# Performance work log

Measured on AMD Instinct MI355X. Metric: run time of the kernel, lower is better.

The kernel has to match this reference:

```python
import jax, jax.numpy as jnp
import numpy as np

N, D, K, V, H, F_ = 4096, 128, 64, 64, 4, 256
EPS = 1e-5


def _layer_norm(x, g, b):
    m = jnp.mean(x, axis=-1, keepdims=True)
    v = jnp.mean((x - m) ** 2, axis=-1, keepdims=True)
    return (x - m) * jax.lax.rsqrt(v + EPS) * g + b


def setup_inputs() -> dict:
    key = jax.random.key(0)
    ks = jax.random.split(key, 20)
    s_in = (2.0 / D) ** 0.5  # kaiming-ish scale for q/k/v projections
    inp = {
        "x": jax.random.normal(ks[0], (N, D), jnp.float32),
        "rpe": jax.random.normal(ks[1], (5, N, N), jnp.float32) * 0.02,
        "Wq": jax.random.normal(ks[2], (H, D, K), jnp.float32) * s_in,
        "bq": jnp.zeros((H, K), jnp.float32),
        "Wk": jax.random.normal(ks[3], (H, D, K), jnp.float32) * s_in,
        "bk": jnp.zeros((H, K), jnp.float32),
        "Wv": jax.random.normal(ks[4], (H, D, V), jnp.float32) * s_in,
        "bv": jnp.zeros((H, V), jnp.float32),
        "rpe_w": jax.random.normal(ks[5], (5,), jnp.float32) * (1.0 / 5.0) ** 0.5,
        "rpe_b": jnp.zeros((), jnp.float32),
        "Wo": jax.random.normal(ks[6], (H * V, D), jnp.float32) * (1.0 / (H * V)) ** 0.5,
        "bo": jnp.zeros((D,), jnp.float32),
        "W1": jax.random.normal(ks[7], (D, F_), jnp.float32) * (1.0 / D) ** 0.5,
        "b1": jnp.zeros((F_,), jnp.float32),
        "W2": jax.random.normal(ks[8], (F_, D), jnp.float32) * (1.0 / F_) ** 0.5,
        "b2": jnp.zeros((D,), jnp.float32),
        "ln1_g": jnp.ones((D,), jnp.float32),
        "ln1_b": jnp.zeros((D,), jnp.float32),
        "ln2_g": jnp.ones((D,), jnp.float32),
        "ln2_b": jnp.zeros((D,), jnp.float32),
    }
    return inp


def reference(x, rpe, Wq, bq, Wk, bk, Wv, bv, rpe_w, rpe_b, Wo, bo,
              W1, b1, W2, b2, ln1_g, ln1_b, ln2_g, ln2_b):
    # ReLU'd per-head projections (vectorized over heads): [H, N, K/V]
    q = jax.nn.relu(jnp.einsum("nd,hdk->hnk", x, Wq) + bq[:, None, :])
    k = jax.nn.relu(jnp.einsum("nd,hdk->hnk", x, Wk) + bk[:, None, :])
    v = jax.nn.relu(jnp.einsum("nd,hdv->hnv", x, Wv) + bv[:, None, :])
    scores = jnp.einsum("hnk,hmk->hnm", q, k) / jnp.sqrt(jnp.asarray(K, x.dtype))
    attn = jax.nn.softmax(scores, axis=-1)  # torch dim=1 on 2D == last axis
    o = jnp.einsum("hnm,hmv->hnv", attn, v)
    mho = jnp.transpose(o, (1, 0, 2)).reshape(N, H * V)  # concat heads
    # RPE: Linear(5->1) over channel axis -> [N, N], then left-matmul
    rpe_weights = jnp.einsum("fnm,f->nm", rpe, rpe_w) + rpe_b
    adjusted = rpe_weights @ mho
    proj = adjusted @ Wo + bo
    x1 = _layer_norm(x + proj, ln1_g, ln1_b)  # dropout is identity (eval)
    ffn = jax.nn.relu(x1 @ W1 + b1) @ W2 + b2
    return _layer_norm(x1 + ffn, ln2_g, ln2_b)
```

## Files before the change

kernel.cpp:

```cpp
#include <hip/hip_runtime.h>

typedef __attribute__((ext_vector_type(8))) short bf16x8;
typedef __attribute__((ext_vector_type(4))) float f32x4;

#define N_TOK 4096
#define NC_ATT 4
#define NC_GEMM 8

static __device__ __forceinline__ ushort f2bf(float f) {
    union { float f; unsigned u; } x; x.f = f;
    unsigned u = x.u;
    unsigned r = (u + 0x7FFFu + ((u >> 16) & 1u)) >> 16;
    return (ushort)r;
}
static __device__ __forceinline__ unsigned pkbf(float a, float b) {
    return (unsigned)f2bf(a) | ((unsigned)f2bf(b) << 16);
}

__global__ void prep_all(const float* __restrict__ x,
                         const float* __restrict__ Wq, const float* __restrict__ Wk,
                         const float* __restrict__ Wv, const float* __restrict__ Wo,
                         const float* __restrict__ W1, const float* __restrict__ W2,
                         ushort* __restrict__ xb, ushort* __restrict__ WqT,
                         ushort* __restrict__ WkT, ushort* __restrict__ WvT,
                         ushort* __restrict__ WoT, ushort* __restrict__ W1T,
                         ushort* __restrict__ W2T) {
    int i = blockIdx.x * 256 + threadIdx.x;
    if (i < 131072) {
        float4 v = ((const float4*)x)[i];
        ushort4 o;
        o.x = f2bf(v.x); o.y = f2bf(v.y); o.z = f2bf(v.z); o.w = f2bf(v.w);
        ((ushort4*)xb)[i] = o;
        return;
    }
    int j = i - 131072;
    int t = j >> 15, e = j & 32767;
    if (t < 3) {
        const float* src = (t == 0 ? Wq : t == 1 ? Wk : Wv);
        ushort* dst = (t == 0 ? WqT : t == 1 ? WkT : WvT);
        int h = e >> 13, rem = e & 8191, d = rem >> 6, k = rem & 63;
        dst[h * 8192 + k * 128 + d] = f2bf(src[e]);
    } else if (t == 3) {
        int r = e >> 7, c = e & 127;
        WoT[c * 256 + r] = f2bf(Wo[e]);
    } else if (t == 4) {
        int r = e >> 8, c = e & 255;
        W1T[c * 128 + r] = f2bf(W1[e]);
    } else {
        int r = e >> 7, c = e & 127;
        W2T[c * 256 + r] = f2bf(W2[e]);
    }
}

__global__ __launch_bounds__(256) void qkv_proj(
    const ushort* __restrict__ xb, const ushort* __restrict__ WqT,
    const ushort* __restrict__ WkT, const ushort* __restrict__ WvT,
    const float* __restrict__ bq, const float* __restrict__ bk, const float* __restrict__ bv,
    ushort* __restrict__ qb, ushort* __restrict__ kb, ushort* __restrict__ vT) {
    int m0 = blockIdx.x * 64;
    int h = blockIdx.y & 3, which = blockIdx.y >> 2;
    int wave = threadIdx.x >> 6, lane = threadIdx.x & 63;
    int fr = lane & 15, kg = lane >> 4;
    int wm = m0 + wave * 16;
    const ushort* WT = (which == 0 ? WqT : which == 1 ? WkT : WvT) + (long)h * 64 * 128;
    const float* bias = (which == 0 ? bq : which == 1 ? bk : bv) + h * 64;
    f32x4 acc[4] = {};
    for (int k0 = 0; k0 < 128; k0 += 32) {
        bf16x8 a = *(const bf16x8*)(xb + (long)(wm + fr) * 128 + k0 + kg * 8);
#pragma unroll
        for (int t = 0; t < 4; ++t) {
            bf16x8 b = *(const bf16x8*)(WT + (long)(t * 16 + fr) * 128 + k0 + kg * 8);
            acc[t] = __builtin_amdgcn_mfma_f32_16x16x32_bf16(a, b, acc[t], 0, 0, 0);
        }
    }
    int rb = wm + kg * 4;
#pragma unroll
    for (int t = 0; t < 4; ++t) {
        int col = t * 16 + fr;
        float bs = bias[col];
        if (which == 2) {
            ushort4 o;
            o.x = f2bf(fmaxf(acc[t][0] + bs, 0.f));
            o.y = f2bf(fmaxf(acc[t][1] + bs, 0.f));
            o.z = f2bf(fmaxf(acc[t][2] + bs, 0.f));
            o.w = f2bf(fmaxf(acc[t][3] + bs, 0.f));
            *(ushort4*)(vT + ((long)h * 64 + col) * N_TOK + rb) = o;
        } else {
            ushort* dst = (which == 0 ? qb : kb) + (long)h * N_TOK * 64;
            float scl = (which == 0) ? 0.125f : 1.0f;
#pragma unroll
            for (int r = 0; r < 4; ++r)
                dst[(long)(rb + r) * 64 + col] = f2bf(fmaxf(acc[t][r] + bs, 0.f) * scl);
        }
    }
}

__global__ __launch_bounds__(256) void attn_flash2(
    const ushort* __restrict__ qb, const ushort* __restrict__ kb,
    const ushort* __restrict__ vT, float* __restrict__ opart,
    float* __restrict__ mlpart) {
    int qt = blockIdx.x, h = blockIdx.y, cz = blockIdx.z;
    int w = threadIdx.x >> 6, lane = threadIdx.x & 63;
    int fr = lane & 15, kg = lane >> 4;
    int lr = lane >> 3, lc = lane & 7;
    int swz = (lc ^ (lr & 7)) * 8;
    __shared__ ushort Kt[2][64 * 64];
    __shared__ ushort Vt[2][64 * 64];
    __shared__ ushort Pl[4][16 * 64];
    const ushort* qh = qb + (long)h * N_TOK * 64;
    const ushort* kh = kb + (long)h * N_TOK * 64;
    const ushort* vh = vT + (long)h * 64 * N_TOK;
    int q0 = qt * 64 + w * 16;
    bf16x8 qf0 = *(const bf16x8*)(qh + (long)(q0 + fr) * 64 + kg * 8);
    bf16x8 qf1 = *(const bf16x8*)(qh + (long)(q0 + fr) * 64 + 32 + kg * 8);
    f32x4 o[4] = {};
    float mrun = -1e30f, lrun = 0.f;
    int nbase = cz * (N_TOK / NC_ATT);
    auto stage = [&](int buf, int s) {
        int n0 = nbase + s * 64;
#pragma unroll
        for (int j = 0; j < 2; ++j) {
            int i = w * 2 + j;
            int row = i * 8 + lr;
            __builtin_amdgcn_global_load_lds(
                (const __attribute__((address_space(1))) unsigned int*)(kh + (long)(n0 + row) * 64 + swz),
                (__attribute__((address_space(3))) unsigned int*)(&Kt[buf][i * 512]), 16, 0, 0);
        }
#pragma unroll
        for (int j = 0; j < 2; ++j) {
            int i = w * 2 + j;
            int row = i * 8 + lr;
            __builtin_amdgcn_global_load_lds(
                (const __attribute__((address_space(1))) unsigned int*)(vh + (long)row * N_TOK + n0 + swz),
                (__attribute__((address_space(3))) unsigned int*)(&Vt[buf][i * 512]), 16, 0, 0);
        }
    };
    stage(0, 0);
    __syncthreads();
    const int NS = (N_TOK / NC_ATT) / 64;
    for (int s = 0; s < NS; ++s) {
        int buf = s & 1;
        if (s + 1 < NS) stage(buf ^ 1, s + 1);
        f32x4 sc[4] = {};
#pragma unroll
        for (int t = 0; t < 4; ++t) {
            int row = t * 16 + fr;
            bf16x8 k0 = *(const bf16x8*)(&Kt[buf][row * 64 + ((kg * 8) ^ ((row & 7) * 8))]);
            bf16x8 k1 = *(const bf16x8*)(&Kt[buf][row * 64 + ((32 + kg * 8) ^ ((row & 7) * 8))]);
            sc[t] = __builtin_amdgcn_mfma_f32_16x16x32_bf16(k0, qf0, sc[t], 0, 0, 0);
            sc[t] = __builtin_amdgcn_mfma_f32_16x16x32_bf16(k1, qf1, sc[t], 0, 0, 0);
        }
        float mx = sc[0][0];
#pragma unroll
        for (int t = 0; t < 4; ++t)
#pragma unroll
            for (int r = 0; r < 4; ++r) mx = fmaxf(mx, sc[t][r]);
        mx = fmaxf(mx, __shfl_xor(mx, 16));
        mx = fmaxf(mx, __shfl_xor(mx, 32));
        float mnew = fmaxf(mrun, mx);
        float alpha = __expf(mrun - mnew);
        float rs = 0.f;
#pragma unroll
        for (int t = 0; t < 4; ++t)
#pragma unroll
            for (int r = 0; r < 4; ++r) {
                float p = __expf(sc[t][r] - mnew);
                sc[t][r] = p;
                rs += p;
            }
        rs += __shfl_xor(rs, 16);
        rs += __shfl_xor(rs, 32);
        lrun = lrun * alpha + rs;
        mrun = mnew;
        float aq[4];
#pragma unroll
        for (int r = 0; r < 4; ++r) aq[r] = __shfl(alpha, kg * 4 + r);
#pragma unroll
        for (int t = 0; t < 4; ++t)
#pragma unroll
            for (int r = 0; r < 4; ++r) o[t][r] *= aq[r];
#pragma unroll
        for (int t = 0; t < 4; ++t) {
            uint2 u;
            u.x = pkbf(sc[t][0], sc[t][1]);
            u.y = pkbf(sc[t][2], sc[t][3]);
            *(uint2*)(&Pl[w][fr * 64 + ((t * 16 + kg * 4) ^ ((fr & 7) * 8))]) = u;
        }
#pragma unroll
        for (int ks = 0; ks < 2; ++ks) {
            bf16x8 pf = *(const bf16x8*)(&Pl[w][fr * 64 + ((ks * 32 + kg * 8) ^ ((fr & 7) * 8))]);
#pragma unroll
            for (int t = 0; t < 4; ++t) {
                int row = t * 16 + fr;
                bf16x8 b = *(const bf16x8*)(&Vt[buf][row * 64 + ((ks * 32 + kg * 8) ^ ((row & 7) * 8))]);
                o[t] = __builtin_amdgcn_mfma_f32_16x16x32_bf16(pf, b, o[t], 0, 0, 0);
            }
        }
        __syncthreads();
    }
    float linv = 1.0f / lrun;
    float lq[4];
#pragma unroll
    for (int r = 0; r < 4; ++r) lq[r] = __shfl(linv, kg * 4 + r);
    float* ob = opart + (((long)cz * 4 + h) * N_TOK + q0 + kg * 4) * 64;
#pragma unroll
    for (int t = 0; t < 4; ++t)
#pragma unroll
        for (int r = 0; r < 4; ++r)
            ob[(long)r * 64 + t * 16 + fr] = o[t][r] * lq[r];
    if (lane < 16) {
        float* mlb = mlpart + (((long)cz * 4 + h) * N_TOK + q0 + lane) * 2;
        mlb[0] = mrun;
        mlb[1] = lrun;
    }
}

__global__ __launch_bounds__(256) void attn_combine(
    const float* __restrict__ opart, const float* __restrict__ mlpart,
    ushort* __restrict__ mho) {
    int h = blockIdx.y;
    int q0 = blockIdx.x * 64;
    int tid = threadIdx.x;
    int ql = tid >> 4, qv = tid & 15;
#pragma unroll
    for (int pass = 0; pass < 4; ++pass) {
        int q = q0 + pass * 16 + ql;
        float m[NC_ATT], l[NC_ATT], M = -1e30f;
#pragma unroll
        for (int c = 0; c < NC_ATT; ++c) {
            const float* mlb = mlpart + (((long)c * 4 + h) * N_TOK + q) * 2;
            m[c] = mlb[0]; l[c] = mlb[1];
            M = fmaxf(M, m[c]);
        }
        float L = 0.f, wgt[NC_ATT];
#pragma unroll
        for (int c = 0; c < NC_ATT; ++c) { wgt[c] = __expf(m[c] - M); L += l[c] * wgt[c]; }
        float inv = 1.0f / L;
#pragma unroll
        for (int c = 0; c < NC_ATT; ++c) wgt[c] *= l[c] * inv;
        float ax = 0.f, ay = 0.f, az = 0.f, aw = 0.f;
#pragma unroll
        for (int c = 0; c < NC_ATT; ++c) {
            float4 v = *(const float4*)(opart + (((long)c * 4 + h) * N_TOK + q) * 64 + qv * 4);
            ax += v.x * wgt[c]; ay += v.y * wgt[c]; az += v.z * wgt[c]; aw += v.w * wgt[c];
        }
        ushort4 o;
        o.x = f2bf(ax); o.y = f2bf(ay); o.z = f2bf(az); o.w = f2bf(aw);
        *(ushort4*)(mho + (long)q * 256 + h * 64 + qv * 4) = o;
    }
}

__global__ __launch_bounds__(256) void gemm_bt_plain(
    const ushort* __restrict__ A, const ushort* __restrict__ BT,
    ushort* __restrict__ outp, int Ncols, int Kd) {
    int m0 = blockIdx.x * 64, n0 = blockIdx.y * 64;
    int wave = threadIdx.x >> 6, lane = threadIdx.x & 63;
    int fr = lane & 15, kg = lane >> 4;
    int wm = m0 + wave * 16;
    f32x4 acc[4] = {};
    for (int k0 = 0; k0 < Kd; k0 += 32) {
        bf16x8 a = *(const bf16x8*)(A + (long)(wm + fr) * Kd + k0 + kg * 8);
#pragma unroll
        for (int t = 0; t < 4; ++t) {
            bf16x8 b = *(const bf16x8*)(BT + (long)(n0 + t * 16 + fr) * Kd + k0 + kg * 8);
            acc[t] = __builtin_amdgcn_mfma_f32_16x16x32_bf16(a, b, acc[t], 0, 0, 0);
        }
    }
    int rb = wm + kg * 4;
#pragma unroll
    for (int t = 0; t < 4; ++t) {
        int col = n0 + t * 16 + fr;
#pragma unroll
        for (int r = 0; r < 4; ++r)
            outp[(long)(rb + r) * Ncols + col] = f2bf(acc[t][r]);
    }
}

__global__ __launch_bounds__(512) void gemm_big_fused(
    const float* __restrict__ rpe, const float* __restrict__ rpe_w,
    const float* __restrict__ rpe_b, const ushort* __restrict__ PT,
    float* __restrict__ part) {
    int mt = blockIdx.x, cz = blockIdx.y;
    int tid = threadIdx.x;
    int w = tid >> 6, lane = tid & 63;
    int fr = lane & 15, kg = lane >> 4;
    int lr = lane >> 3, lc = lane & 7;
    int swz = (lc ^ (lr & 7)) * 8;
    int ms = w >> 1, nh = w & 1;
    __shared__ ushort Bt[2][128 * 64];
    __shared__ ushort At[2][64 * 64];
    int m0 = mt * 64;
    long kbase = (long)cz * (N_TOK / NC_GEMM);
    float w0 = rpe_w[0], w1 = rpe_w[1], w2 = rpe_w[2], w3 = rpe_w[3], w4 = rpe_w[4];
    float bb = rpe_b[0];
    auto stage_B = [&](int buf, int s) {
        const ushort* src = PT + kbase + s * 64 + swz;
#pragma unroll
        for (int j = 0; j < 2; ++j) {
            int i = w * 2 + j;
            int row = i * 8 + lr;
            __builtin_amdgcn_global_load_lds(
                (const __attribute__((address_space(1))) unsigned int*)(src + (long)row * N_TOK),
                (__attribute__((address_space(3))) unsigned int*)(&Bt[buf][i * 512]), 16, 0, 0);
        }
    };
    float4 pA[10];
    auto load_A = [&](int s) {
        const float* base = rpe + (long)m0 * N_TOK + kbase + s * 64;
#pragma unroll
        for (int rnd = 0; rnd < 2; ++rnd) {
            int idx = tid + rnd * 512;
            int row = idx >> 4, c4 = (idx & 15) * 4;
            const float* pr = base + (long)row * N_TOK + c4;
#pragma unroll
            for (int pl = 0; pl < 5; ++pl)
                pA[rnd * 5 + pl] = *(const float4*)(pr + (long)pl * ((long)N_TOK * N_TOK));
        }
    };
    auto write_A = [&](int buf) {
#pragma unroll
        for (int rnd = 0; rnd < 2; ++rnd) {
            int idx = tid + rnd * 512;
            int row = idx >> 4, c4 = (idx & 15) * 4;
            float4 p0 = pA[rnd * 5], p1 = pA[rnd * 5 + 1], p2 = pA[rnd * 5 + 2];
            float4 p3 = pA[rnd * 5 + 3], p4 = pA[rnd * 5 + 4];
            float v0 = bb + w0 * p0.x + w1 * p1.x + w2 * p2.x + w3 * p3.x + w4 * p4.x;
            float v1 = bb + w0 * p0.y + w1 * p1.y + w2 * p2.y + w3 * p3.y + w4 * p4.y;
            float v2 = bb + w0 * p0.z + w1 * p1.z + w2 * p2.z + w3 * p3.z + w4 * p4.z;
            float v3 = bb + w0 * p0.w + w1 * p1.w + w2 * p2.w + w3 * p3.w + w4 * p4.w;
            uint2 u;
            u.x = pkbf(v0, v1);
            u.y = pkbf(v2, v3);
            *(uint2*)(&At[buf][row * 64 + (c4 ^ ((row & 7) * 8))]) = u;
        }
    };
    f32x4 acc[4] = {};
    load_A(0);
    stage_B(0, 0);
    write_A(0);
    __syncthreads();
    const int NS = (N_TOK / NC_GEMM) / 64;
    int arow = ms * 16 + fr;
    for (int s = 0; s < NS; ++s) {
        int buf = s & 1;
        if (s + 1 < NS) { stage_B(buf ^ 1, s + 1); load_A(s + 1); }
#pragma unroll
        for (int ks = 0; ks < 2; ++ks) {
            bf16x8 av = *(const bf16x8*)(&At[buf][arow * 64 + ((ks * 32 + kg * 8) ^ ((arow & 7) * 8))]);
#pragma unroll
            for (int nf = 0; nf < 4; ++nf) {
                int row = nh * 64 + nf * 16 + fr;
                bf16x8 b = *(const bf16x8*)(&Bt[buf][row * 64 + ((ks * 32 + kg * 8) ^ ((row & 7) * 8))]);
                acc[nf] = __builtin_amdgcn_mfma_f32_16x16x32_bf16(av, b, acc[nf], 0, 0, 0);
            }
        }
        if (s + 1 < NS) write_A(buf ^ 1);
        __syncthreads();
    }
    float* pb = part + ((long)cz * N_TOK + m0 + ms * 16 + kg * 4) * 128 + nh * 64 + fr;
#pragma unroll
    for (int nf = 0; nf < 4; ++nf)
#pragma unroll
        for (int r = 0; r < 4; ++r)
            pb[(long)r * 128 + nf * 16] = acc[nf][r];
}

__global__ __launch_bounds__(256) void megatail(
    const float* __restrict__ gpart, const float* __restrict__ bo,
    const float* __restrict__ x, const float* __restrict__ g1,
    const float* __restrict__ lb1, const ushort* __restrict__ W1T,
    const float* __restrict__ b1, const ushort* __restrict__ W2T,
    const float* __restrict__ b2, const float* __restrict__ g2,
    const float* __restrict__ lb2, float* __restrict__ out) {
    int r0 = blockIdx.x * 16;
    int tid = threadIdx.x;
    int w = tid >> 6, lane = tid & 63;
    int fr = lane & 15, kg = lane >> 4;
    __shared__ float x1f[16][132];
    __shared__ ushort x1b[16][128];
    __shared__ ushort hbuf[16][256];
    __shared__ float otile[16][132];
    int row = tid >> 4, c0 = (tid & 15) * 8;
    {
        float v[8];
        float4 s0 = {0.f, 0.f, 0.f, 0.f}, s1 = {0.f, 0.f, 0.f, 0.f};
#pragma unroll
        for (int c = 0; c < NC_GEMM; ++c) {
            const float* pr = gpart + ((long)c * N_TOK + r0 + row) * 128 + c0;
            float4 a = *(const float4*)(pr);
            float4 b = *(const float4*)(pr + 4);
            s0.x += a.x; s0.y += a.y; s0.z += a.z; s0.w += a.w;
            s1.x += b.x; s1.y += b.y; s1.z += b.z; s1.w += b.w;
        }
        const float* xr = x + (long)(r0 + row) * 128 + c0;
        v[0] = s0.x + bo[c0 + 0] + xr[0];
        v[1] = s0.y + bo[c0 + 1] + xr[1];
        v[2] = s0.z + bo[c0 + 2] + xr[2];
        v[3] = s0.w + bo[c0 + 3] + xr[3];
        v[4] = s1.x + bo[c0 + 4] + xr[4];
        v[5] = s1.y + bo[c0 + 5] + xr[5];
        v[6] = s1.z + bo[c0 + 6] + xr[6];
        v[7] = s1.w + bo[c0 + 7] + xr[7];
        float s = 0.f;
#pragma unroll
        for (int jj = 0; jj < 8; ++jj) s += v[jj];
#pragma unroll
        for (int off = 1; off < 16; off <<= 1) s += __shfl_xor(s, off);
        float mean = s * (1.0f / 128.0f);
        float ss = 0.f;
#pragma unroll
        for (int jj = 0; jj < 8; ++jj) { float d = v[jj] - mean; ss += d * d; }
#pragma unroll
        for (int off = 1; off < 16; off <<= 1) ss += __shfl_xor(ss, off);
        float rstd = rsqrtf(ss * (1.0f / 128.0f) + 1e-5f);
        union { bf16x8 vec; ushort us[8]; } pk8;
#pragma unroll
        for (int jj = 0; jj < 8; ++jj) {
            float y = (v[jj] - mean) * rstd * g1[c0 + jj] + lb1[c0 + jj];
            x1f[row][c0 + jj] = y;
            pk8.us[jj] = f2bf(y);
        }
        *(bf16x8*)(&x1b[row][c0 ^ ((row & 7) * 8)]) = pk8.vec;
    }
    __syncthreads();
    {
        f32x4 a1[4] = {};
#pragma unroll
        for (int ks = 0; ks < 4; ++ks) {
            bf16x8 a = *(const bf16x8*)(&x1b[fr][(ks * 32 + kg * 8) ^ ((fr & 7) * 8)]);
#pragma unroll
            for (int t = 0; t < 4; ++t) {
                bf16x8 b = *(const bf16x8*)(W1T + (long)(w * 64 + t * 16 + fr) * 128 + ks * 32 + kg * 8);
                a1[t] = __builtin_amdgcn_mfma_f32_16x16x32_bf16(a, b, a1[t], 0, 0, 0);
            }
        }
#pragma unroll
        for (int t = 0; t < 4; ++t) {
            int col = w * 64 + t * 16 + fr;
            float bs = b1[col];
#pragma unroll
            for (int r = 0; r < 4; ++r) {
                int rr = kg * 4 + r;
                hbuf[rr][col ^ ((rr & 7) * 8)] = f2bf(fmaxf(a1[t][r] + bs, 0.f));
            }
        }
    }
    __syncthreads();
    {
        f32x4 a2[2] = {};
#pragma unroll
        for (int ks = 0; ks < 8; ++ks) {
            bf16x8 a = *(const bf16x8*)(&hbuf[fr][(ks * 32 + kg * 8) ^ ((fr & 7) * 8)]);
#pragma unroll
            for (int t = 0; t < 2; ++t) {
                bf16x8 b = *(const bf16x8*)(W2T + (long)(w * 32 + t * 16 + fr) * 256 + ks * 32 + kg * 8);
                a2[t] = __builtin_amdgcn_mfma_f32_16x16x32_bf16(a, b, a2[t], 0, 0, 0);
            }
        }
#pragma unroll
        for (int t = 0; t < 2; ++t) {
            int col = w * 32 + t * 16 + fr;
            float bs = b2[col];
#pragma unroll
            for (int r = 0; r < 4; ++r) {
                int rr = kg * 4 + r;
                otile[rr][col] = a2[t][r] + bs + x1f[rr][col];
            }
        }
    }
    __syncthreads();
    {
        float v[8];
        float s = 0.f;
#pragma unroll
        for (int jj = 0; jj < 8; ++jj) { v[jj] = otile[row][c0 + jj]; s += v[jj]; }
#pragma unroll
        for (int off = 1; off < 16; off <<= 1) s += __shfl_xor(s, off);
        float mean = s * (1.0f / 128.0f);
        float ss = 0.f;
#pragma unroll
        for (int jj = 0; jj < 8; ++jj) { float d = v[jj] - mean; ss += d * d; }
#pragma unroll
        for (int off = 1; off < 16; off <<= 1) ss += __shfl_xor(ss, off);
        float rstd = rsqrtf(ss * (1.0f / 128.0f) + 1e-5f);
#pragma unroll
        for (int jj = 0; jj < 8; ++jj) {
            float y = (v[jj] - mean) * rstd * g2[c0 + jj] + lb2[c0 + jj];
            out[(long)(r0 + row) * 128 + c0 + jj] = y;
        }
    }
}

extern "C" void kernel_launch(void* const* d_in, const int* in_sizes, int n_in,
                              void* d_out, int out_size, void* d_ws, size_t ws_size,
                              hipStream_t stream) {
    const float* x     = (const float*)d_in[0];
    const float* rpe   = (const float*)d_in[1];
    const float* Wq    = (const float*)d_in[2];
    const float* bq    = (const float*)d_in[3];
    const float* Wk    = (const float*)d_in[4];
    const float* bk    = (const float*)d_in[5];
    const float* Wv    = (const float*)d_in[6];
    const float* bv    = (const float*)d_in[7];
    const float* rpe_w = (const float*)d_in[8];
    const float* rpe_b = (const float*)d_in[9];
    const float* Wo    = (const float*)d_in[10];
    const float* bo    = (const float*)d_in[11];
    const float* W1    = (const float*)d_in[12];
    const float* b1    = (const float*)d_in[13];
    const float* W2    = (const float*)d_in[14];
    const float* b2    = (const float*)d_in[15];
    const float* g1    = (const float*)d_in[16];
    const float* lb1   = (const float*)d_in[17];
    const float* g2    = (const float*)d_in[18];
    const float* lb2   = (const float*)d_in[19];

    char* wp = (char*)d_ws;
    auto alloc = [&](size_t sz) { char* p = wp; wp += (sz + 255) & ~(size_t)255; return p; };
    ushort* xb    = (ushort*)alloc((size_t)4096 * 128 * 2);
    ushort* WqT   = (ushort*)alloc((size_t)4 * 64 * 128 * 2);
    ushort* WkT   = (ushort*)alloc((size_t)4 * 64 * 128 * 2);
    ushort* WvT   = (ushort*)alloc((size_t)4 * 64 * 128 * 2);
    ushort* WoT   = (ushort*)alloc((size_t)128 * 256 * 2);
    ushort* W1T   = (ushort*)alloc((size_t)256 * 128 * 2);
    ushort* W2T   = (ushort*)alloc((size_t)128 * 256 * 2);
    ushort* qb    = (ushort*)alloc((size_t)4 * 4096 * 64 * 2);
    ushort* kbuf  = (ushort*)alloc((size_t)4 * 4096 * 64 * 2);
    ushort* vT    = (ushort*)alloc((size_t)4 * 64 * 4096 * 2);
    ushort* mho   = (ushort*)alloc((size_t)4096 * 256 * 2);
    ushort* PTb   = (ushort*)alloc((size_t)128 * 4096 * 2);
    float*  opart = (float*)alloc((size_t)NC_ATT * 4 * 4096 * 64 * 4);
    float*  mlprt = (float*)alloc((size_t)NC_ATT * 4 * 4096 * 2 * 4);
    float*  gpart = (float*)alloc((size_t)NC_GEMM * 4096 * 128 * 4);

    prep_all<<<1280, 256, 0, stream>>>(x, Wq, Wk, Wv, Wo, W1, W2,
                                       xb, WqT, WkT, WvT, WoT, W1T, W2T);
    qkv_proj<<<dim3(64, 12), 256, 0, stream>>>(xb, WqT, WkT, WvT, bq, bk, bv, qb, kbuf, vT);
    attn_flash2<<<dim3(64, 4, NC_ATT), 256, 0, stream>>>(qb, kbuf, vT, opart, mlprt);
    attn_combine<<<dim3(64, 4), 256, 0, stream>>>(opart, mlprt, mho);
    gemm_bt_plain<<<dim3(2, 64), 256, 0, stream>>>(WoT, mho, PTb, 4096, 256);
    gemm_big_fused<<<dim3(64, NC_GEMM), 512, 0, stream>>>(rpe, rpe_w, rpe_b, PTb, gpart);
    megatail<<<256, 256, 0, stream>>>(gpart, bo, x, g1, lb1, W1T, b1, W2T, b2,
                                      g2, lb2, (float*)d_out);
}
```

Measured before the change: 152.4 us.

## Fuse attention combine with Wo projection, store partials in bf16, lazy rescale

The attention split-combine and the Wo projection GEMM are merged into one kernel. It combines the per-chunk partials into a swizzled LDS tile and runs the MFMA against WoT directly, so the intermediate mho buffer and one launch go away. Attention partial outputs are now stored as bf16 instead of fp32, halving that traffic. The flash loop folds log2(e) into the q scale to use exp2f, and only rescales the accumulators when the running max grows by more than 8. This trades some precision (bf16 partials, p values up to 2^8) for fewer exp and multiply operations.

```diff
diff --git a/kernel.cpp b/kernel.cpp
--- a/kernel.cpp
+++ b/kernel.cpp
@@ -15,6 +15,9 @@
 }
 static __device__ __forceinline__ unsigned pkbf(float a, float b) {
     return (unsigned)f2bf(a) | ((unsigned)f2bf(b) << 16);
+}
+static __device__ __forceinline__ float bf2f(ushort u) {
+    union { unsigned u; float f; } x; x.u = (unsigned)u << 16; return x.f;
 }
 
 __global__ void prep_all(const float* __restrict__ x,
@@ -87,7 +90,7 @@
             *(ushort4*)(vT + ((long)h * 64 + col) * N_TOK + rb) = o;
         } else {
             ushort* dst = (which == 0 ? qb : kb) + (long)h * N_TOK * 64;
-            float scl = (which == 0) ? 0.125f : 1.0f;
+            float scl = (which == 0) ? 0.125f * 1.44269504f : 1.0f;
 #pragma unroll
             for (int r = 0; r < 4; ++r)
                 dst[(long)(rb + r) * 64 + col] = f2bf(fmaxf(acc[t][r] + bs, 0.f) * scl);
@@ -97,7 +100,7 @@
 
 __global__ __launch_bounds__(256) void attn_flash2(
     const ushort* __restrict__ qb, const ushort* __restrict__ kb,
-    const ushort* __restrict__ vT, float* __restrict__ opart,
+    const ushort* __restrict__ vT, ushort* __restrict__ opart,
     float* __restrict__ mlpart) {
     int qt = blockIdx.x, h = blockIdx.y, cz = blockIdx.z;
     int w = threadIdx.x >> 6, lane = threadIdx.x & 63;
@@ -157,28 +160,31 @@
             for (int r = 0; r < 4; ++r) mx = fmaxf(mx, sc[t][r]);
         mx = fmaxf(mx, __shfl_xor(mx, 16));
         mx = fmaxf(mx, __shfl_xor(mx, 32));
-        float mnew = fmaxf(mrun, mx);
-        float alpha = __expf(mrun - mnew);
+        if (__any(mx - mrun > 8.f)) {
+            float mnew = fmaxf(mrun, mx);
+            float alpha = exp2f(mrun - mnew);
+            lrun *= alpha;
+            mrun = mnew;
+            float aq[4];
+#pragma unroll
+            for (int r = 0; r < 4; ++r) aq[r] = __shfl(alpha, kg * 4 + r);
+#pragma unroll
+            for (int t = 0; t < 4; ++t)
+#pragma unroll
+                for (int r = 0; r < 4; ++r) o[t][r] *= aq[r];
+        }
         float rs = 0.f;
 #pragma unroll
         for (int t = 0; t < 4; ++t)
 #pragma unroll
             for (int r = 0; r < 4; ++r) {
-                float p = __expf(sc[t][r] - mnew);
+                float p = exp2f(sc[t][r] - mrun);
                 sc[t][r] = p;
                 rs += p;
             }
         rs += __shfl_xor(rs, 16);
         rs += __shfl_xor(rs, 32);
-        lrun = lrun * alpha + rs;
-        mrun = mnew;
-        float aq[4];
-#pragma unroll
-        for (int r = 0; r < 4; ++r) aq[r] = __shfl(alpha, kg * 4 + r);
-#pragma unroll
-        for (int t = 0; t < 4; ++t)
-#pragma unroll
-            for (int r = 0; r < 4; ++r) o[t][r] *= aq[r];
+        lrun += rs;
 #pragma unroll
         for (int t = 0; t < 4; ++t) {
             uint2 u;
@@ -202,12 +208,12 @@
     float lq[4];
 #pragma unroll
     for (int r = 0; r < 4; ++r) lq[r] = __shfl(linv, kg * 4 + r);
-    float* ob = opart + (((long)cz * 4 + h) * N_TOK + q0 + kg * 4) * 64;
+    ushort* ob = opart + (((long)cz * 4 + h) * N_TOK + q0 + kg * 4) * 64;
 #pragma unroll
     for (int t = 0; t < 4; ++t)
 #pragma unroll
         for (int r = 0; r < 4; ++r)
-            ob[(long)r * 64 + t * 16 + fr] = o[t][r] * lq[r];
+            ob[(long)r * 64 + t * 16 + fr] = f2bf(o[t][r] * lq[r]);
     if (lane < 16) {
         float* mlb = mlpart + (((long)cz * 4 + h) * N_TOK + q0 + lane) * 2;
         mlb[0] = mrun;
@@ -215,64 +221,80 @@
     }
 }
 
-__global__ __launch_bounds__(256) void attn_combine(
-    const float* __restrict__ opart, const float* __restrict__ mlpart,
-    ushort* __restrict__ mho) {
-    int h = blockIdx.y;
+__global__ __launch_bounds__(256) void combine_wo(
+    const ushort* __restrict__ opart, const float* __restrict__ mlpart,
+    const ushort* __restrict__ WoT, ushort* __restrict__ PT) {
     int q0 = blockIdx.x * 64;
     int tid = threadIdx.x;
-    int ql = tid >> 4, qv = tid & 15;
-#pragma unroll
-    for (int pass = 0; pass < 4; ++pass) {
-        int q = q0 + pass * 16 + ql;
-        float m[NC_ATT], l[NC_ATT], M = -1e30f;
-#pragma unroll
-        for (int c = 0; c < NC_ATT; ++c) {
-            const float* mlb = mlpart + (((long)c * 4 + h) * N_TOK + q) * 2;
-            m[c] = mlb[0]; l[c] = mlb[1];
-            M = fmaxf(M, m[c]);
-        }
-        float L = 0.f, wgt[NC_ATT];
-#pragma unroll
-        for (int c = 0; c < NC_ATT; ++c) { wgt[c] = __expf(m[c] - M); L += l[c] * wgt[c]; }
-        float inv = 1.0f / L;
-#pragma unroll
-        for (int c = 0; c < NC_ATT; ++c) wgt[c] *= l[c] * inv;
-        float ax = 0.f, ay = 0.f, az = 0.f, aw = 0.f;
-#pragma unroll
-        for (int c = 0; c < NC_ATT; ++c) {
-            float4 v = *(const float4*)(opart + (((long)c * 4 + h) * N_TOK + q) * 64 + qv * 4);
-            ax += v.x * wgt[c]; ay += v.y * wgt[c]; az += v.z * wgt[c]; aw += v.w * wgt[c];
-        }
-        ushort4 o;
-        o.x = f2bf(ax); o.y = f2bf(ay); o.z = f2bf(az); o.w = f2bf(aw);
-        *(ushort4*)(mho + (long)q * 256 + h * 64 + qv * 4) = o;
-    }
-}
-
-__global__ __launch_bounds__(256) void gemm_bt_plain(
-    const ushort* __restrict__ A, const ushort* __restrict__ BT,
-    ushort* __restrict__ outp, int Ncols, int Kd) {
-    int m0 = blockIdx.x * 64, n0 = blockIdx.y * 64;
-    int wave = threadIdx.x >> 6, lane = threadIdx.x & 63;
-    int fr = lane & 15, kg = lane >> 4;
-    int wm = m0 + wave * 16;
-    f32x4 acc[4] = {};
-    for (int k0 = 0; k0 < Kd; k0 += 32) {
-        bf16x8 a = *(const bf16x8*)(A + (long)(wm + fr) * Kd + k0 + kg * 8);
-#pragma unroll
-        for (int t = 0; t < 4; ++t) {
-            bf16x8 b = *(const bf16x8*)(BT + (long)(n0 + t * 16 + fr) * Kd + k0 + kg * 8);
-            acc[t] = __builtin_amdgcn_mfma_f32_16x16x32_bf16(a, b, acc[t], 0, 0, 0);
-        }
-    }
-    int rb = wm + kg * 4;
-#pragma unroll
-    for (int t = 0; t < 4; ++t) {
-        int col = n0 + t * 16 + fr;
-#pragma unroll
-        for (int r = 0; r < 4; ++r)
-            outp[(long)(rb + r) * Ncols + col] = f2bf(acc[t][r]);
+    __shared__ ushort mt[64 * 256];
+    {
+        int q = tid >> 2, vg = tid & 3;
+        long qg = q0 + q;
+#pragma unroll
+        for (int h = 0; h < 4; ++h) {
+            float m[NC_ATT], l[NC_ATT], M = -1e30f;
+#pragma unroll
+            for (int c = 0; c < NC_ATT; ++c) {
+                const float* mlb = mlpart + (((long)c * 4 + h) * N_TOK + qg) * 2;
+                m[c] = mlb[0]; l[c] = mlb[1];
+                M = fmaxf(M, m[c]);
+            }
+            float L = 0.f, co[NC_ATT];
+#pragma unroll
+            for (int c = 0; c < NC_ATT; ++c) { co[c] = exp2f(m[c] - M) * l[c]; L += co[c]; }
+            float inv = 1.0f / L;
+#pragma unroll
+            for (int c = 0; c < NC_ATT; ++c) co[c] *= inv;
+            float a[16];
+#pragma unroll
+            for (int j = 0; j < 16; ++j) a[j] = 0.f;
+#pragma unroll
+            for (int c = 0; c < NC_ATT; ++c) {
+                const ushort* pr = opart + (((long)c * 4 + h) * N_TOK + qg) * 64 + vg * 16;
+                bf16x8 v0 = *(const bf16x8*)(pr);
+                bf16x8 v1 = *(const bf16x8*)(pr + 8);
+#pragma unroll
+                for (int j = 0; j < 8; ++j) {
+                    a[j] += co[c] * bf2f((ushort)v0[j]);
+                    a[8 + j] += co[c] * bf2f((ushort)v1[j]);
+                }
+            }
+            int c0 = h * 64 + vg * 16;
+            uint2 u0, u1;
+            u0.x = pkbf(a[0], a[1]); u0.y = pkbf(a[2], a[3]);
+            u1.x = pkbf(a[4], a[5]); u1.y = pkbf(a[6], a[7]);
+            *(uint2*)(&mt[q * 256 + (c0 ^ ((q & 7) * 8))]) = u0;
+            *(uint2*)(&mt[q * 256 + ((c0 + 4) ^ ((q & 7) * 8))]) = u1;
+            u0.x = pkbf(a[8], a[9]); u0.y = pkbf(a[10], a[11]);
+            u1.x = pkbf(a[12], a[13]); u1.y = pkbf(a[14], a[15]);
+            *(uint2*)(&mt[q * 256 + ((c0 + 8) ^ ((q & 7) * 8))]) = u0;
+            *(uint2*)(&mt[q * 256 + ((c0 + 12) ^ ((q & 7) * 8))]) = u1;
+        }
+    }
+    __syncthreads();
+    {
+        int w = tid >> 6, lane = tid & 63;
+        int fr = lane & 15, kg = lane >> 4;
+        f32x4 acc[2][4] = {};
+        for (int k0 = 0; k0 < 256; k0 += 32) {
+            bf16x8 a0 = *(const bf16x8*)(WoT + (long)(w * 32 + fr) * 256 + k0 + kg * 8);
+            bf16x8 a1 = *(const bf16x8*)(WoT + (long)(w * 32 + 16 + fr) * 256 + k0 + kg * 8);
+#pragma unroll
+            for (int qt = 0; qt < 4; ++qt) {
+                int row = qt * 16 + fr;
+                bf16x8 b = *(const bf16x8*)(&mt[row * 256 + ((k0 + kg * 8) ^ ((row & 7) * 8))]);
+                acc[0][qt] = __builtin_amdgcn_mfma_f32_16x16x32_bf16(a0, b, acc[0][qt], 0, 0, 0);
+                acc[1][qt] = __builtin_amdgcn_mfma_f32_16x16x32_bf16(a1, b, acc[1][qt], 0, 0, 0);
+            }
+        }
+#pragma unroll
+        for (int dt = 0; dt < 2; ++dt)
+#pragma unroll
+            for (int qt = 0; qt < 4; ++qt)
+#pragma unroll
+                for (int r = 0; r < 4; ++r)
+                    PT[(long)(w * 32 + dt * 16 + kg * 4 + r) * N_TOK + q0 + qt * 16 + fr] =
+                        f2bf(acc[dt][qt][r]);
     }
 }
 
@@ -527,9 +549,8 @@
     ushort* qb    = (ushort*)alloc((size_t)4 * 4096 * 64 * 2);
     ushort* kbuf  = (ushort*)alloc((size_t)4 * 4096 * 64 * 2);
     ushort* vT    = (ushort*)alloc((size_t)4 * 64 * 4096 * 2);
-    ushort* mho   = (ushort*)alloc((size_t)4096 * 256 * 2);
     ushort* PTb   = (ushort*)alloc((size_t)128 * 4096 * 2);
-    float*  opart = (float*)alloc((size_t)NC_ATT * 4 * 4096 * 64 * 4);
+    ushort* opart = (ushort*)alloc((size_t)NC_ATT * 4 * 4096 * 64 * 2);
     float*  mlprt = (float*)alloc((size_t)NC_ATT * 4 * 4096 * 2 * 4);
     float*  gpart = (float*)alloc((size_t)NC_GEMM * 4096 * 128 * 4);
 
@@ -537,8 +558,7 @@
                                        xb, WqT, WkT, WvT, WoT, W1T, W2T);
     qkv_proj<<<dim3(64, 12), 256, 0, stream>>>(xb, WqT, WkT, WvT, bq, bk, bv, qb, kbuf, vT);
     attn_flash2<<<dim3(64, 4, NC_ATT), 256, 0, stream>>>(qb, kbuf, vT, opart, mlprt);
-    attn_combine<<<dim3(64, 4), 256, 0, stream>>>(opart, mlprt, mho);
-    gemm_bt_plain<<<dim3(2, 64), 256, 0, stream>>>(WoT, mho, PTb, 4096, 256);
+    combine_wo<<<64, 256, 0, stream>>>(opart, mlprt, WoT, PTb);
     gemm_big_fused<<<dim3(64, NC_GEMM), 512, 0, stream>>>(rpe, rpe_w, rpe_b, PTb, gpart);
     megatail<<<256, 256, 0, stream>>>(gpart, bo, x, g1, lb1, W1T, b1, W2T, b2,
                                       g2, lb2, (float*)d_out);
```

Measured after the change: 151.6 us. No clear change (-0.6%).
